# Performance work log

Hardware: AMD Instinct MI355X
Metric: run time of the kernel (lower is better)

## Reference

```python
import jax, jax.numpy as jnp
import numpy as np

H = 16          # bit depth
N_K = 2         # random masks per flipped bit
TP = 8          # location dims per node
CUR_TP = 4      # dims updated per step
CUR_PORTION = 0.8
N = 1 << H      # location value range
T = 1024        # stations
S = 64          # neighbors per station
D = 256         # embedding dim
C = 2 * H * N_K + 1  # candidate locations per station


def _cos_sim(a, b):
    # frexp-based integer 'cosine' similarity from CritiGraph.cos_similarity
    sg = jnp.where(a >= 0, 1.0, -1.0) * jnp.where(b >= 0, 1.0, -1.0)
    x = ((jnp.abs(a) ^ jnp.abs(b)) + 1).astype(jnp.float32)
    _, e = jnp.frexp(x)  # exponent = bit length of (xor+1)
    return sg * (1.0 - e.astype(jnp.float32) / H)


def _connection(ori, rand_numbers):
    # ori: [T,tp] int64, rand_numbers: [T,H,N_K,tp] int64 in [0, N)
    bits = jnp.int64(1) << jnp.arange(H, dtype=jnp.int64)          # [H]
    flipped = ori[:, None, :] ^ bits[None, :, None]                # [T,H,tp]
    masks = rand_numbers & (bits - 1)[None, :, None, None]        # low-k-bit masks
    res = (flipped[:, :, None, :] ^ masks).reshape(ori.shape[0], H * N_K, TP)
    # candidate order: flipped variants, original (index H*N_K ... wait: res has H*N_K), original, negated
    return jnp.concatenate([res, ori[:, None, :], -res], axis=1)  # [T,C,tp]


def setup_inputs() -> dict:
    key = jax.random.key(0)
    ks = jax.random.split(key, 8)
    return {
        "sta_loc": jax.random.randint(ks[0], (T, TP), 1 - N, N, dtype=jnp.int64),
        "nei_loc": jax.random.randint(ks[1], (T, S, TP), 1 - N, N, dtype=jnp.int64),
        "rand_numbers": jax.random.randint(ks[2], (T, H, N_K, TP), 0, N, dtype=jnp.int64),
        "sta_emb": jax.random.normal(ks[3], (T, D), dtype=jnp.float32),
        "nei_emb": jax.random.normal(ks[4], (T, S, D), dtype=jnp.float32),
        "mask": (jax.random.uniform(ks[5], (T, S)) > 0.1).astype(jnp.float32),
        "rand_vals": jax.random.uniform(ks[6], (T, TP), dtype=jnp.float32),
        "t_rand": jax.random.uniform(ks[7], (T,), dtype=jnp.float32),
    }


def _forward(sta_loc, nei_loc, rand_numbers, sta_emb, nei_emb, mask, rand_vals, t_rand):
    cnc_loc = _connection(sta_loc, rand_numbers)                    # [T,C,tp]
    # euclidean-space cosine targets
    sta_n = sta_emb / jnp.linalg.norm(sta_emb, axis=-1, keepdims=True)
    nei_n = nei_emb / jnp.linalg.norm(nei_emb, axis=-1, keepdims=True)
    eu_val = jnp.einsum("td,tsd->ts", sta_n, nei_n)                 # [T,S]
    # ct_val swap-one-dim kernel (= ct_val_triton math)
    cos_sn = _cos_sim(sta_loc[:, None, :], nei_loc)                 # [T,S,tp]
    cos_sn_sum = cos_sn.sum(axis=-1)                                # [T,S]
    cos_cn = _cos_sim(cnc_loc[:, None, :, :], nei_loc[:, :, None, :])  # [T,S,C,tp]
    ct_val = (cos_sn_sum[:, :, None, None] - cos_sn[:, :, None, :] + cos_cn) / TP
    # masked squared cosine loss (loom_valid)
    lth = mask.sum(axis=1) + 1e-12                                  # [T]
    eu = eu_val[:, :, None, None]
    loss = jnp.square(ct_val - eu) * jnp.abs(eu) * mask[:, :, None, None]
    loss = loss.sum(axis=1) / lth[:, None, None]                    # [T,C,tp]
    # get_best_loc argmin routing
    argmin_all = jnp.argmin(loss, axis=1)                           # [T,tp]
    base = jnp.full((T, TP), H * N_K, dtype=argmin_all.dtype)       # index of original loc
    rand_cols = jnp.argsort(rand_vals, axis=1)[:, :CUR_TP]          # [T,cur_tp]
    sel = t_rand < CUR_PORTION                                      # [T]
    rows = jnp.broadcast_to(jnp.arange(T)[:, None], (T, CUR_TP))
    upd = jnp.where(sel[:, None], argmin_all[rows, rand_cols], base[rows, rand_cols])
    cnc_idx = base.at[rows, rand_cols].set(upd)                     # [T,tp]
    ti = jnp.arange(T)[:, None]
    di = jnp.arange(TP)[None, :]
    selected_locs = cnc_loc[ti, cnc_idx, di]                        # [T,tp]
    real_loss = loss[ti, cnc_idx, di].mean(axis=-1)                 # [T]
    return selected_locs, real_loss


def reference(sta_loc, nei_loc, rand_numbers, sta_emb, nei_emb, mask, rand_vals, t_rand):
    return _forward(sta_loc, nei_loc, rand_numbers, sta_emb, nei_emb, mask, rand_vals, t_rand)
```

## Files before the change

### kernel.cpp

```cpp
#include <hip/hip_runtime.h>
#include <math.h>

#define T_  1024
#define S_  64
#define D_  256
#define TP_ 8
#define H_  16
#define C_  65
#define CUR_TP_ 4

__device__ __forceinline__ float cos_sim_i(int a, int b) {
    float sg = ((a >= 0) == (b >= 0)) ? 1.0f : -1.0f;
    int aa = a < 0 ? -a : a;
    int bb = b < 0 ? -b : b;
    int x = (aa ^ bb) + 1;
    int e = 32 - __clz(x);
    return sg * (1.0f - (float)e * 0.0625f);
}

__device__ __forceinline__ int cnc_val(int c, int sl, const int* rn_row, int p) {
    if (c == 32) return sl;
    int cc = (c < 32) ? c : (c - 33);
    int h = cc >> 1, k = cc & 1;
    int m = rn_row[h * 16 + k * 8 + p] & ((1 << h) - 1);
    int v = (sl ^ (1 << h)) ^ m;
    return (c < 32) ? v : -v;
}

__global__ __launch_bounds__(256) void critigraph_kernel(
    const int* __restrict__ sta_loc,
    const int* __restrict__ nei_loc,
    const int* __restrict__ rand_numbers,
    const float* __restrict__ sta_emb,
    const float* __restrict__ nei_emb,
    const float* __restrict__ mask,
    const float* __restrict__ rand_vals,
    const float* __restrict__ t_rand,
    float* __restrict__ out_sel,
    float* __restrict__ out_loss)
{
    const int t = blockIdx.x;
    const int tid = threadIdx.x;
    const int lane = tid & 63;
    const int wave = tid >> 6;

    __shared__ __align__(16) float s_sta[D_];
    __shared__ int   s_nl[S_ * TP_];
    __shared__ int   s_rn[H_ * 2 * TP_];
    __shared__ int   s_sl[TP_];
    __shared__ float s_m[S_];
    __shared__ float s_eu[S_];
    __shared__ float s_w[S_];
    __shared__ float s_cs[S_ * TP_];
    __shared__ float s_css[S_];
    __shared__ float s_loss[C_ * TP_];
    __shared__ float s_red[4];
    __shared__ float s_inv;
    __shared__ float s_lth;
    __shared__ int   s_cidx[TP_];

    s_sta[tid] = sta_emb[t * D_ + tid];
    s_nl[tid]       = nei_loc[t * S_ * TP_ + tid];
    s_nl[tid + 256] = nei_loc[t * S_ * TP_ + tid + 256];
    s_rn[tid] = rand_numbers[t * 256 + tid];
    if (tid < TP_) s_sl[tid] = sta_loc[t * TP_ + tid];
    if (tid < S_)  s_m[tid]  = mask[t * S_ + tid];
    __syncthreads();

    {
        float v = s_sta[tid];
        float sq = v * v;
        for (int off = 32; off; off >>= 1) sq += __shfl_xor(sq, off, 64);
        if (lane == 0) s_red[wave] = sq;
    }
    __syncthreads();
    if (tid == 0) {
        float tot = s_red[0] + s_red[1] + s_red[2] + s_red[3];
        s_inv = 1.0f / sqrtf(tot);
        float c = 0.f;
        for (int s = 0; s < S_; s++) c += s_m[s];
        s_lth = c + 1e-12f;
    }
    __syncthreads();

    {
        float4 sv = reinterpret_cast<const float4*>(s_sta)[lane];
        const float4* nrow = reinterpret_cast<const float4*>(nei_emb + (size_t)t * S_ * D_);
        for (int i = 0; i < 16; i++) {
            int s = wave * 16 + i;
            float4 nv = nrow[s * (D_ / 4) + lane];
            float d0 = nv.x * sv.x + nv.y * sv.y + nv.z * sv.z + nv.w * sv.w;
            float n0 = nv.x * nv.x + nv.y * nv.y + nv.z * nv.z + nv.w * nv.w;
            for (int off = 32; off; off >>= 1) {
                d0 += __shfl_xor(d0, off, 64);
                n0 += __shfl_xor(n0, off, 64);
            }
            if (lane == 0) {
                float eu = d0 * s_inv * (1.0f / sqrtf(n0));
                s_eu[s] = eu;
                s_w[s]  = fabsf(eu) * s_m[s];
            }
        }
    }

    for (int q = tid; q < S_ * TP_; q += 256) {
        int p = q & 7;
        s_cs[q] = cos_sim_i(s_sl[p], s_nl[q]);
    }
    __syncthreads();
    if (tid < S_) {
        float a = 0.f;
        for (int p = 0; p < TP_; p++) a += s_cs[tid * 8 + p];
        s_css[tid] = a;
    }
    __syncthreads();

    for (int q = tid; q < C_ * TP_; q += 256) {
        int c = q >> 3, p = q & 7;
        int v = cnc_val(c, s_sl[p], s_rn, p);
        float acc = 0.f;
        for (int s = 0; s < S_; s++) {
            float cc = cos_sim_i(v, s_nl[s * 8 + p]);
            float ct = (s_css[s] - s_cs[s * 8 + p] + cc) * 0.125f;
            float d = ct - s_eu[s];
            acc += d * d * s_w[s];
        }
        s_loss[q] = acc / s_lth;
    }
    __syncthreads();

    if (tid < TP_) {
        float best = s_loss[tid];
        int bi = 0;
        for (int c = 1; c < C_; c++) {
            float v = s_loss[c * 8 + tid];
            if (v < best) { best = v; bi = c; }
        }
        s_cidx[tid] = bi;
    }
    __syncthreads();

    if (tid == 0) {
        float rv[TP_];
        int am[TP_], cidx[TP_];
        bool taken[TP_];
        for (int p = 0; p < TP_; p++) {
            rv[p] = rand_vals[t * TP_ + p];
            am[p] = s_cidx[p];
            cidx[p] = 32;
            taken[p] = false;
        }
        bool sel = t_rand[t] < 0.8f;
        for (int j = 0; j < CUR_TP_; j++) {
            int bi = -1; float bv = 0.f;
            for (int p = 0; p < TP_; p++) {
                if (taken[p]) continue;
                if (bi < 0 || rv[p] < bv) { bi = p; bv = rv[p]; }
            }
            taken[bi] = true;
            cidx[bi] = sel ? am[bi] : 32;
        }
        for (int p = 0; p < TP_; p++) s_cidx[p] = cidx[p];
    }
    __syncthreads();

    if (tid < TP_) {
        int c = s_cidx[tid];
        int v = cnc_val(c, s_sl[tid], s_rn, tid);
        out_sel[t * TP_ + tid] = (float)v;
    }
    if (tid == 64) {
        float a = 0.f;
        for (int p = 0; p < TP_; p++) a += s_loss[s_cidx[p] * 8 + p];
        out_loss[t] = a * 0.125f;
    }
}

extern "C" void kernel_launch(void* const* d_in, const int* in_sizes, int n_in,
                              void* d_out, int out_size, void* d_ws, size_t ws_size,
                              hipStream_t stream) {
    const int*   sta_loc      = (const int*)d_in[0];
    const int*   nei_loc      = (const int*)d_in[1];
    const int*   rand_numbers = (const int*)d_in[2];
    const float* sta_emb      = (const float*)d_in[3];
    const float* nei_emb      = (const float*)d_in[4];
    const float* mask         = (const float*)d_in[5];
    const float* rand_vals    = (const float*)d_in[6];
    const float* t_rand       = (const float*)d_in[7];

    float* out_sel  = (float*)d_out;
    float* out_loss = out_sel + T_ * TP_;

    critigraph_kernel<<<T_, 256, 0, stream>>>(
        sta_loc, nei_loc, rand_numbers, sta_emb, nei_emb, mask,
        rand_vals, t_rand, out_sel, out_loss);
}
```

Measured before the change: 136.3 us.

## Share cos-sim between negated candidates and prefetch neighbor embeddings into registers

After: 113.4 us. 16.8% less time.

```diff
diff --git a/kernel.cpp b/kernel.cpp
--- a/kernel.cpp
+++ b/kernel.cpp
@@ -5,9 +5,16 @@
 #define S_  64
 #define D_  256
 #define TP_ 8
-#define H_  16
 #define C_  65
-#define CUR_TP_ 4
+
+__device__ __forceinline__ int cnc_val(int c, int sl, const int* rn_row, int p) {
+    if (c == 32) return sl;
+    int cc = (c < 32) ? c : (c - 33);
+    int h = cc >> 1, k = cc & 1;
+    int m = rn_row[h * 16 + k * 8 + p] & ((1 << h) - 1);
+    int v = (sl ^ (1 << h)) ^ m;
+    return (c < 32) ? v : -v;
+}
 
 __device__ __forceinline__ float cos_sim_i(int a, int b) {
     float sg = ((a >= 0) == (b >= 0)) ? 1.0f : -1.0f;
@@ -18,16 +25,7 @@
     return sg * (1.0f - (float)e * 0.0625f);
 }
 
-__device__ __forceinline__ int cnc_val(int c, int sl, const int* rn_row, int p) {
-    if (c == 32) return sl;
-    int cc = (c < 32) ? c : (c - 33);
-    int h = cc >> 1, k = cc & 1;
-    int m = rn_row[h * 16 + k * 8 + p] & ((1 << h) - 1);
-    int v = (sl ^ (1 << h)) ^ m;
-    return (c < 32) ? v : -v;
-}
-
-__global__ __launch_bounds__(256) void critigraph_kernel(
+__global__ __launch_bounds__(256, 4) void critigraph_kernel(
     const int* __restrict__ sta_loc,
     const int* __restrict__ nei_loc,
     const int* __restrict__ rand_numbers,
@@ -45,133 +43,172 @@
     const int wave = tid >> 6;
 
     __shared__ __align__(16) float s_sta[D_];
-    __shared__ int   s_nl[S_ * TP_];
-    __shared__ int   s_rn[H_ * 2 * TP_];
-    __shared__ int   s_sl[TP_];
-    __shared__ float s_m[S_];
-    __shared__ float s_eu[S_];
-    __shared__ float s_w[S_];
-    __shared__ float s_cs[S_ * TP_];
-    __shared__ float s_css[S_];
-    __shared__ float s_loss[C_ * TP_];
+    __shared__ __align__(16) float4 s_cb[512];
+    __shared__ int   s_nl[512];
+    __shared__ int   s_rn[256];
+    __shared__ int   s_sl[8];
+    __shared__ float s_m[64];
+    __shared__ float s_rv[8];
+    __shared__ float s_cs[512];
+    __shared__ float s_css[64];
+    __shared__ float s_eun[64];
+    __shared__ float s_eu[64];
+    __shared__ float s_w[64];
+    __shared__ float s_loss[C_ * 8];
     __shared__ float s_red[4];
-    __shared__ float s_inv;
-    __shared__ float s_lth;
-    __shared__ int   s_cidx[TP_];
-
-    s_sta[tid] = sta_emb[t * D_ + tid];
-    s_nl[tid]       = nei_loc[t * S_ * TP_ + tid];
-    s_nl[tid + 256] = nei_loc[t * S_ * TP_ + tid + 256];
+    __shared__ float s_inv, s_lth;
+    __shared__ int   s_amin[8];
+    __shared__ int   s_cidx[8];
+
+    const int srow = tid >> 2, j4 = tid & 3;
+    const float4* nrow = reinterpret_cast<const float4*>(nei_emb + (size_t)t * S_ * D_);
+    float4 nv[16];
+#pragma unroll
+    for (int i = 0; i < 16; i++) nv[i] = nrow[srow * 64 + i * 4 + j4];
+
+    float stav = sta_emb[t * D_ + tid];
+    s_sta[tid] = stav;
+    s_nl[tid]       = nei_loc[t * 512 + tid];
+    s_nl[tid + 256] = nei_loc[t * 512 + tid + 256];
     s_rn[tid] = rand_numbers[t * 256 + tid];
-    if (tid < TP_) s_sl[tid] = sta_loc[t * TP_ + tid];
-    if (tid < S_)  s_m[tid]  = mask[t * S_ + tid];
+    if (tid < 8) { s_sl[tid] = sta_loc[t * 8 + tid]; s_rv[tid] = rand_vals[t * 8 + tid]; }
+    if (tid < 64) s_m[tid] = mask[t * 64 + tid];
     __syncthreads();
 
     {
-        float v = s_sta[tid];
-        float sq = v * v;
+        s_cs[tid]       = cos_sim_i(s_sl[tid & 7], s_nl[tid]);
+        s_cs[tid + 256] = cos_sim_i(s_sl[tid & 7], s_nl[tid + 256]);
+        float sq = stav * stav;
+#pragma unroll
         for (int off = 32; off; off >>= 1) sq += __shfl_xor(sq, off, 64);
         if (lane == 0) s_red[wave] = sq;
-    }
-    __syncthreads();
+        if (wave == 1) {
+            float mv = s_m[lane];
+#pragma unroll
+            for (int off = 32; off; off >>= 1) mv += __shfl_xor(mv, off, 64);
+            if (lane == 0) s_lth = mv + 1e-12f;
+        }
+    }
+    __syncthreads();
+
+    if (tid == 0) s_inv = 1.0f / sqrtf(s_red[0] + s_red[1] + s_red[2] + s_red[3]);
+    if (tid < 64) {
+        float a = s_cs[tid * 8];
+        for (int p = 1; p < 8; p++) a += s_cs[tid * 8 + p];
+        s_css[tid] = a;
+    }
+    {
+        const float4* st4 = reinterpret_cast<const float4*>(s_sta);
+        float d0 = 0.f, n0 = 0.f;
+#pragma unroll
+        for (int i = 0; i < 16; i++) {
+            float4 sv = st4[i * 4 + j4];
+            float4 nn = nv[i];
+            d0 = fmaf(nn.x, sv.x, d0); d0 = fmaf(nn.y, sv.y, d0);
+            d0 = fmaf(nn.z, sv.z, d0); d0 = fmaf(nn.w, sv.w, d0);
+            n0 = fmaf(nn.x, nn.x, n0); n0 = fmaf(nn.y, nn.y, n0);
+            n0 = fmaf(nn.z, nn.z, n0); n0 = fmaf(nn.w, nn.w, n0);
+        }
+        d0 += __shfl_xor(d0, 1, 64); d0 += __shfl_xor(d0, 2, 64);
+        n0 += __shfl_xor(n0, 1, 64); n0 += __shfl_xor(n0, 2, 64);
+        if (j4 == 0) s_eun[srow] = d0 * (1.0f / sqrtf(n0));
+    }
+    __syncthreads();
+
+#pragma unroll
+    for (int q = tid; q < 512; q += 256) {
+        int s = q >> 3;
+        int nl = s_nl[q];
+        int code = (nl < 0) ? (int)(0x80000000u | (unsigned)(-nl)) : nl;
+        float g = s_css[s] - s_cs[q];
+        float eu = s_eun[s] * s_inv;
+        float w = fabsf(eu) * s_m[s];
+        s_cb[q] = make_float4(__int_as_float(code), g, eu, w);
+        if ((q & 7) == 0) { s_eu[s] = eu; s_w[s] = w; }
+    }
+    __syncthreads();
+
+    {
+        const float lth = s_lth;
+        const int c = tid >> 3, p = tid & 7;
+        int v = cnc_val(c, s_sl[p], s_rn, p);
+        unsigned avc  = (v < 0) ? (0x80000000u | (unsigned)(-v)) : (unsigned)v;
+        unsigned flip = (v != 0) ? 0x80000000u : 0u;
+        float acc1 = 0.f, acc2 = 0.f;
+#pragma unroll 4
+        for (int s = 0; s < 64; s++) {
+            float4 cb = s_cb[s * 8 + p];
+            unsigned y = avc ^ (unsigned)__float_as_int(cb.x);
+            int x = (int)(y & 0x7fffffffu) + 1;
+            float ccu = fmaf((float)__clz(x), 0.0625f, -1.0f);
+            unsigned ccb = __float_as_uint(ccu) ^ (y & 0x80000000u);
+            float cc1 = __uint_as_float(ccb);
+            float cc2 = __uint_as_float(ccb ^ flip);
+            float d1 = fmaf(cb.y + cc1, 0.125f, -cb.z);
+            float d2 = fmaf(cb.y + cc2, 0.125f, -cb.z);
+            acc1 = fmaf(d1 * d1, cb.w, acc1);
+            acc2 = fmaf(d2 * d2, cb.w, acc2);
+        }
+        s_loss[c * 8 + p]        = acc1 / lth;
+        s_loss[(c + 33) * 8 + p] = acc2 / lth;
+        if (tid < 8) {
+            float a32 = 0.f;
+            for (int s = 0; s < 64; s++) {
+                float d = fmaf(s_css[s], 0.125f, -s_eu[s]);
+                a32 = fmaf(d * d, s_w[s], a32);
+            }
+            s_loss[256 + tid] = a32 / lth;
+        }
+    }
+    __syncthreads();
+
+    if (tid < 64) {
+        const int p = tid >> 3, g = tid & 7;
+        float bv = s_loss[g * 8 + p];
+        int bi = g;
+        for (int k = 1; k < 8; k++) {
+            int c = g + 8 * k;
+            float vv = s_loss[c * 8 + p];
+            if (vv < bv) { bv = vv; bi = c; }
+        }
+        if (g == 0) {
+            float vv = s_loss[512 + p];
+            if (vv < bv) { bv = vv; bi = 64; }
+        }
+#pragma unroll
+        for (int off = 1; off < 8; off <<= 1) {
+            float ov = __shfl_xor(bv, off, 64);
+            int   oi = __shfl_xor(bi, off, 64);
+            if (ov < bv || (ov == bv && oi < bi)) { bv = ov; bi = oi; }
+        }
+        if (g == 0) s_amin[p] = bi;
+    }
+    __syncthreads();
+
     if (tid == 0) {
-        float tot = s_red[0] + s_red[1] + s_red[2] + s_red[3];
-        s_inv = 1.0f / sqrtf(tot);
-        float c = 0.f;
-        for (int s = 0; s < S_; s++) c += s_m[s];
-        s_lth = c + 1e-12f;
-    }
-    __syncthreads();
-
-    {
-        float4 sv = reinterpret_cast<const float4*>(s_sta)[lane];
-        const float4* nrow = reinterpret_cast<const float4*>(nei_emb + (size_t)t * S_ * D_);
-        for (int i = 0; i < 16; i++) {
-            int s = wave * 16 + i;
-            float4 nv = nrow[s * (D_ / 4) + lane];
-            float d0 = nv.x * sv.x + nv.y * sv.y + nv.z * sv.z + nv.w * sv.w;
-            float n0 = nv.x * nv.x + nv.y * nv.y + nv.z * nv.z + nv.w * nv.w;
-            for (int off = 32; off; off >>= 1) {
-                d0 += __shfl_xor(d0, off, 64);
-                n0 += __shfl_xor(n0, off, 64);
-            }
-            if (lane == 0) {
-                float eu = d0 * s_inv * (1.0f / sqrtf(n0));
-                s_eu[s] = eu;
-                s_w[s]  = fabsf(eu) * s_m[s];
-            }
-        }
-    }
-
-    for (int q = tid; q < S_ * TP_; q += 256) {
-        int p = q & 7;
-        s_cs[q] = cos_sim_i(s_sl[p], s_nl[q]);
-    }
-    __syncthreads();
-    if (tid < S_) {
-        float a = 0.f;
-        for (int p = 0; p < TP_; p++) a += s_cs[tid * 8 + p];
-        s_css[tid] = a;
-    }
-    __syncthreads();
-
-    for (int q = tid; q < C_ * TP_; q += 256) {
-        int c = q >> 3, p = q & 7;
-        int v = cnc_val(c, s_sl[p], s_rn, p);
-        float acc = 0.f;
-        for (int s = 0; s < S_; s++) {
-            float cc = cos_sim_i(v, s_nl[s * 8 + p]);
-            float ct = (s_css[s] - s_cs[s * 8 + p] + cc) * 0.125f;
-            float d = ct - s_eu[s];
-            acc += d * d * s_w[s];
-        }
-        s_loss[q] = acc / s_lth;
-    }
-    __syncthreads();
-
-    if (tid < TP_) {
-        float best = s_loss[tid];
-        int bi = 0;
-        for (int c = 1; c < C_; c++) {
-            float v = s_loss[c * 8 + tid];
-            if (v < best) { best = v; bi = c; }
-        }
-        s_cidx[tid] = bi;
-    }
-    __syncthreads();
-
-    if (tid == 0) {
-        float rv[TP_];
-        int am[TP_], cidx[TP_];
-        bool taken[TP_];
-        for (int p = 0; p < TP_; p++) {
-            rv[p] = rand_vals[t * TP_ + p];
-            am[p] = s_cidx[p];
-            cidx[p] = 32;
-            taken[p] = false;
-        }
         bool sel = t_rand[t] < 0.8f;
-        for (int j = 0; j < CUR_TP_; j++) {
-            int bi = -1; float bv = 0.f;
-            for (int p = 0; p < TP_; p++) {
+        float rv[8]; int cidx[8]; bool taken[8];
+        for (int p = 0; p < 8; p++) { rv[p] = s_rv[p]; cidx[p] = 32; taken[p] = false; }
+        for (int j = 0; j < 4; j++) {
+            int bi = -1; float bvv = 0.f;
+            for (int p = 0; p < 8; p++) {
                 if (taken[p]) continue;
-                if (bi < 0 || rv[p] < bv) { bi = p; bv = rv[p]; }
+                if (bi < 0 || rv[p] < bvv) { bi = p; bvv = rv[p]; }
             }
             taken[bi] = true;
-            cidx[bi] = sel ? am[bi] : 32;
-        }
-        for (int p = 0; p < TP_; p++) s_cidx[p] = cidx[p];
-    }
-    __syncthreads();
-
-    if (tid < TP_) {
+            cidx[bi] = sel ? s_amin[bi] : 32;
+        }
+        for (int p = 0; p < 8; p++) s_cidx[p] = cidx[p];
+    }
+    __syncthreads();
+
+    if (tid < 8) {
         int c = s_cidx[tid];
-        int v = cnc_val(c, s_sl[tid], s_rn, tid);
-        out_sel[t * TP_ + tid] = (float)v;
+        out_sel[t * 8 + tid] = (float)cnc_val(c, s_sl[tid], s_rn, tid);
     }
     if (tid == 64) {
         float a = 0.f;
-        for (int p = 0; p < TP_; p++) a += s_loss[s_cidx[p] * 8 + p];
+        for (int p = 0; p < 8; p++) a += s_loss[s_cidx[p] * 8 + p];
         out_loss[t] = a * 0.125f;
     }
 }
```
